# Performance work log

Hardware: AMD Instinct MI355X
Metric: run time of the kernel (lower is better)

Reference implementation:

```python
import jax, jax.numpy as jnp
import numpy as np

B, N, C, K, RPE = 8, 4096, 256, 16, 64
LN_EPS = 1e-5


def _layernorm(x, g, b):
    m = jnp.mean(x, axis=-1, keepdims=True)
    v = jnp.mean((x - m) ** 2, axis=-1, keepdims=True)
    return (x - m) * jax.lax.rsqrt(v + LN_EPS) * g + b


def setup_inputs() -> dict:
    key = jax.random.key(0)
    ks = jax.random.split(key, 10)
    def w(k, shape, s=0.02):
        return jax.random.normal(k, shape, jnp.float32) * s
    return {
        "x": jax.random.normal(ks[0], (B, N, C), jnp.float32),
        "pos": jax.random.normal(ks[1], (B, N, 3), jnp.float32),
        "Wq": w(ks[2], (C, C)),
        "Wk": w(ks[3], (C, C)),
        "Wv": w(ks[4], (C, C)),
        "W1": w(ks[5], (3, RPE)), "b1": jnp.zeros((RPE,), jnp.float32),
        "W2": w(ks[6], (RPE, C)), "b2": jnp.zeros((C,), jnp.float32),
        "Wp": w(ks[7], (C, C)), "bp": jnp.zeros((C,), jnp.float32),
        "gq": jnp.ones((C,), jnp.float32), "betaq": jnp.zeros((C,), jnp.float32),
        "gkv": jnp.ones((C,), jnp.float32), "betakv": jnp.zeros((C,), jnp.float32),
    }


def reference(x, pos, Wq, Wk, Wv, W1, b1, W2, b2, Wp, bp, gq, betaq, gkv, betakv):
    scale = C ** (-0.5)
    x_q = _layernorm(x, gq, betaq)
    x_kv = _layernorm(x, gkv, betakv)
    q = x_q @ Wq                      # (B,N,C)
    k = x_kv @ Wk                     # (B,N,C)
    v = x_kv @ Wv                     # (B,N,C)

    # kNN over squared pairwise distances (self has distance 0 on the diagonal)
    a2 = jnp.sum(pos * pos, axis=-1)                       # (B,N)
    dist2 = a2[:, :, None] + a2[:, None, :] - 2.0 * jnp.einsum(
        "bnc,bmc->bnm", pos, pos)                          # (B,N,N)
    dist2 = jnp.maximum(dist2, 0.0)
    eye = jnp.eye(N, dtype=bool)
    dist2 = jnp.where(eye[None], 0.0, dist2)
    _, idx = jax.lax.top_k(-dist2, K)                      # (B,N,K) smallest-k

    gather = jax.vmap(lambda f, i: f[i])                   # (N,C),(N,K)->(N,K,C)
    k_nb = gather(k, idx)                                  # (B,N,K,C)
    v_nb = gather(v, idx)                                  # (B,N,K,C)
    pos_nb = gather(pos, idx)                              # (B,N,K,3)

    rel = pos[:, :, None, :] - pos_nb                      # (B,N,K,3)
    rel_enc = jax.nn.relu(rel @ W1 + b1) @ W2 + b2         # (B,N,K,C)

    attn_logits = jnp.einsum("bnc,bnkc->bnk", q, k_nb) * scale
    attn_logits = attn_logits + jnp.sum(rel_enc, axis=-1) * scale
    attn = jax.nn.softmax(attn_logits, axis=-1)            # (B,N,K)

    out = jnp.einsum("bnk,bnkc->bnc", attn, v_nb)
    out = out @ Wp + bp
    return out
```

## Files before the change

kernel.cpp:

```cpp
#include <hip/hip_runtime.h>
#include <hip/hip_bf16.h>
#include <stdint.h>

#define Bv 8
#define Nv 4096
#define Cv 256
#define Kv 16
#define RPEv 64
#define CAPv 160

typedef short bf16x8 __attribute__((ext_vector_type(8)));
typedef float f32x4 __attribute__((ext_vector_type(4)));
typedef _Float16 half2v __attribute__((ext_vector_type(2)));
typedef unsigned short u16x2 __attribute__((ext_vector_type(2)));

static __device__ __forceinline__ float bf2f(unsigned int u16) {
    union { unsigned int i; float f; } v; v.i = u16 << 16; return v.f;
}
static __device__ __forceinline__ unsigned short f2bf(float f) {
    union { float f; unsigned int i; } v; v.f = f;
    unsigned int x = v.i;
    return (unsigned short)((x + 0x7fffu + ((x >> 16) & 1u)) >> 16);
}
static __device__ __forceinline__ unsigned int umin32(unsigned int a, unsigned int b) { return a < b ? a : b; }
static __device__ __forceinline__ unsigned int umax32(unsigned int a, unsigned int b) { return a > b ? a : b; }
static __device__ __forceinline__ unsigned short f2h(float f) {
    _Float16 h = (_Float16)f; return __builtin_bit_cast(unsigned short, h);
}
static __device__ __forceinline__ float h2f(unsigned int u) {
    _Float16 h = __builtin_bit_cast(_Float16, (unsigned short)(u & 0xffffu)); return (float)h;
}
static __device__ __forceinline__ half2v bch2(unsigned int u) { return __builtin_bit_cast(half2v, u); }
static __device__ __forceinline__ unsigned int bcu32(u16x2 v) { return __builtin_bit_cast(unsigned int, v); }

__global__ __launch_bounds__(256) void pre_kernel(
    const float* __restrict__ x,
    const float* __restrict__ gq, const float* __restrict__ bq,
    const float* __restrict__ gkv, const float* __restrict__ bkv,
    unsigned short* __restrict__ Aq, unsigned short* __restrict__ Akv,
    const float* __restrict__ Wq, const float* __restrict__ Wk,
    const float* __restrict__ Wv, const float* __restrict__ Wp,
    unsigned short* __restrict__ Bt,
    const float* __restrict__ W2, const float* __restrict__ b2,
    float* __restrict__ w2sum, float* __restrict__ b2sum,
    const float* __restrict__ pos, char* __restrict__ ppos)
{
    const int bid = blockIdx.x;
    const int tid = threadIdx.x;
    if (bid < 4096) {
        const long r0 = (long)bid * 8;
        const int row = tid >> 5;
        const int c0 = (tid & 31) * 8;
        const float* xr = x + (r0 + row) * Cv + c0;
        float xv[8];
        *(float4*)&xv[0] = *(const float4*)xr;
        *(float4*)&xv[4] = *(const float4*)(xr + 4);
        float s = 0.f, s2 = 0.f;
#pragma unroll
        for (int i = 0; i < 8; ++i) { s += xv[i]; s2 = fmaf(xv[i], xv[i], s2); }
#pragma unroll
        for (int m = 16; m >= 1; m >>= 1) { s += __shfl_xor(s, m); s2 += __shfl_xor(s2, m); }
        const float mean = s * (1.f / Cv);
        const float var = fmaf(-mean, mean, s2 * (1.f / Cv));
        const float rs = rsqrtf(fmaxf(var, 0.f) + 1e-5f);
        unsigned int pq[4], pk[4];
#pragma unroll
        for (int i = 0; i < 4; ++i) {
            const int c = c0 + 2 * i;
            const float h0 = (xv[2 * i] - mean) * rs;
            const float h1 = (xv[2 * i + 1] - mean) * rs;
            const unsigned int q0 = f2bf(fmaf(h0, gq[c], bq[c]));
            const unsigned int q1 = f2bf(fmaf(h1, gq[c + 1], bq[c + 1]));
            const unsigned int k0 = f2bf(fmaf(h0, gkv[c], bkv[c]));
            const unsigned int k1 = f2bf(fmaf(h1, gkv[c + 1], bkv[c + 1]));
            pq[i] = q0 | (q1 << 16);
            pk[i] = k0 | (k1 << 16);
        }
        const long off = (r0 + row) * Cv + c0;
        *(uint4*)&Aq[off]  = make_uint4(pq[0], pq[1], pq[2], pq[3]);
        *(uint4*)&Akv[off] = make_uint4(pk[0], pk[1], pk[2], pk[3]);
    } else if (bid < 5120) {
        const int r = bid - 4096;
        const float* W = (r < 256) ? Wq : (r < 512) ? Wk : (r < 768) ? Wv : Wp;
        const int n = r & 255;
        Bt[r * 256 + tid] = f2bf(W[tid * 256 + n]);
    } else if (bid == 5120) {
        if (tid < RPEv) {
            float s = 0.f;
            for (int c = 0; c < Cv; ++c) s += W2[tid * Cv + c];
            w2sum[tid] = s;
        }
        if (tid == 0) {
            float s = 0.f;
            for (int c = 0; c < Cv; ++c) s += b2[c];
            *b2sum = s;
        }
    } else {
        const int b = bid - 5121;
        const float* pb = pos + (size_t)b * Nv * 3;
        uint2* oxy = (uint2*)(ppos + (size_t)b * 24576);
        unsigned int* oz = (unsigned int*)(ppos + (size_t)b * 24576 + 16384);
        for (int i = tid; i < Nv / 2; i += 256) {
            const float* pp = pb + 6 * i;
            const float2 u0 = *(const float2*)pp;
            const float2 u1 = *(const float2*)(pp + 2);
            const float2 u2 = *(const float2*)(pp + 4);
            const unsigned int x0 = f2h(u0.x), y0 = f2h(u0.y), z0 = f2h(u1.x);
            const unsigned int x1 = f2h(u1.y), y1 = f2h(u2.x), z1 = f2h(u2.y);
            oxy[i] = make_uint2(x0 | (x1 << 16), y0 | (y1 << 16));
            oz[i] = z0 | (z1 << 16);
        }
    }
}

__global__ __launch_bounds__(256) void gemm_qkv_kernel(
    const unsigned short* __restrict__ Aq, const unsigned short* __restrict__ Akv,
    const unsigned short* __restrict__ Bt,
    unsigned short* __restrict__ qo, unsigned short* __restrict__ ko,
    unsigned short* __restrict__ vo)
{
    __shared__ unsigned short Albs[2][128 * 64];
    __shared__ unsigned short Blbs[2][128 * 64];

    const int tid = threadIdx.x;
    const int rt = blockIdx.x;
    const int ct = blockIdx.y;
    const unsigned short* A = (ct < 2) ? Aq : Akv;
    const int mat = ct >> 1;
    unsigned short* outp = (mat == 0) ? qo : (mat == 1) ? ko : vo;
    const int colInMat = (ct & 1) * 128;

    const int wid = tid >> 6, l = tid & 63;
    const int wr = wid >> 1, wc = wid & 1;

    int srow[4], scol8[4];
#pragma unroll
    for (int it = 0; it < 4; ++it) {
        const int chunk = it * 256 + tid;
        srow[it] = chunk >> 3;
        scol8[it] = ((chunk & 7) ^ (srow[it] & 7)) * 8;
    }

#define STAGE(buf, ks)                                                                  \
    {                                                                                   \
        _Pragma("unroll")                                                               \
        for (int it = 0; it < 4; ++it) {                                                \
            const unsigned short* ga = A + ((size_t)(rt * 128 + srow[it])) * 256        \
                                         + (ks) * 64 + scol8[it];                       \
            const unsigned short* gb = Bt + ((size_t)(ct * 128 + srow[it])) * 256       \
                                          + (ks) * 64 + scol8[it];                      \
            __builtin_amdgcn_global_load_lds(                                           \
                (const __attribute__((address_space(1))) unsigned int*)(const void*)ga, \
                (__attribute__((address_space(3))) unsigned int*)(void*)                \
                    ((char*)&Albs[buf][0] + (it * 256 + tid) * 16), 16, 0, 0);          \
            __builtin_amdgcn_global_load_lds(                                           \
                (const __attribute__((address_space(1))) unsigned int*)(const void*)gb, \
                (__attribute__((address_space(3))) unsigned int*)(void*)                \
                    ((char*)&Blbs[buf][0] + (it * 256 + tid) * 16), 16, 0, 0);          \
        }                                                                               \
    }

    f32x4 acc[4][4];
#pragma unroll
    for (int m = 0; m < 4; ++m)
#pragma unroll
        for (int n = 0; n < 4; ++n) acc[m][n] = (f32x4){0.f, 0.f, 0.f, 0.f};

    STAGE(0, 0);
    __syncthreads();

    for (int ks = 0; ks < 4; ++ks) {
        const int cur = ks & 1;
        if (ks < 3) STAGE(cur ^ 1, ks + 1);
#pragma unroll
        for (int kk = 0; kk < 2; ++kk) {
            bf16x8 a[4], b[4];
#pragma unroll
            for (int m = 0; m < 4; ++m) {
                const int row = wr * 64 + m * 16 + (l & 15);
                const int byte = row * 128 + ((((kk * 4 + (l >> 4)) * 16)) ^ ((row & 7) << 4));
                a[m] = *(const bf16x8*)((const char*)&Albs[cur][0] + byte);
            }
#pragma unroll
            for (int n = 0; n < 4; ++n) {
                const int row = wc * 64 + n * 16 + (l & 15);
                const int byte = row * 128 + ((((kk * 4 + (l >> 4)) * 16)) ^ ((row & 7) << 4));
                b[n] = *(const bf16x8*)((const char*)&Blbs[cur][0] + byte);
            }
#pragma unroll
            for (int m = 0; m < 4; ++m)
#pragma unroll
                for (int n = 0; n < 4; ++n)
                    acc[m][n] = __builtin_amdgcn_mfma_f32_16x16x32_bf16(a[m], b[n], acc[m][n], 0, 0, 0);
        }
        __syncthreads();
    }

#pragma unroll
    for (int m = 0; m < 4; ++m) {
#pragma unroll
        for (int n = 0; n < 4; ++n) {
#pragma unroll
            for (int j = 0; j < 4; ++j) {
                const int row = rt * 128 + wr * 64 + m * 16 + (l >> 4) * 4 + j;
                const int col = colInMat + wc * 64 + n * 16 + (l & 15);
                outp[(size_t)row * 256 + col] = f2bf(acc[m][n][j]);
            }
        }
    }
#undef STAGE
}

__global__ __launch_bounds__(256) void gemm_proj_kernel(
    const unsigned short* __restrict__ Ab, const unsigned short* __restrict__ Btp,
    const float* __restrict__ bp, float* __restrict__ out)
{
    __shared__ unsigned short Albs[2][128 * 64];
    __shared__ unsigned short Blbs[2][128 * 64];

    const int tid = threadIdx.x;
    const int rt = blockIdx.x;
    const int ct = blockIdx.y;

    const int wid = tid >> 6, l = tid & 63;
    const int wr = wid >> 1, wc = wid & 1;

    int srow[4], scol8[4];
#pragma unroll
    for (int it = 0; it < 4; ++it) {
        const int chunk = it * 256 + tid;
        srow[it] = chunk >> 3;
        scol8[it] = ((chunk & 7) ^ (srow[it] & 7)) * 8;
    }

#define STAGE(buf, ks)                                                                  \
    {                                                                                   \
        _Pragma("unroll")                                                               \
        for (int it = 0; it < 4; ++it) {                                                \
            const unsigned short* ga = Ab + ((size_t)(rt * 128 + srow[it])) * 256       \
                                          + (ks) * 64 + scol8[it];                      \
            const unsigned short* gb = Btp + ((size_t)(ct * 128 + srow[it])) * 256      \
                                           + (ks) * 64 + scol8[it];                     \
            __builtin_amdgcn_global_load_lds(                                           \
                (const __attribute__((address_space(1))) unsigned int*)(const void*)ga, \
                (__attribute__((address_space(3))) unsigned int*)(void*)                \
                    ((char*)&Albs[buf][0] + (it * 256 + tid) * 16), 16, 0, 0);          \
            __builtin_amdgcn_global_load_lds(                                           \
                (const __attribute__((address_space(1))) unsigned int*)(const void*)gb, \
                (__attribute__((address_space(3))) unsigned int*)(void*)                \
                    ((char*)&Blbs[buf][0] + (it * 256 + tid) * 16), 16, 0, 0);          \
        }                                                                               \
    }

    f32x4 acc[4][4];
#pragma unroll
    for (int m = 0; m < 4; ++m)
#pragma unroll
        for (int n = 0; n < 4; ++n) acc[m][n] = (f32x4){0.f, 0.f, 0.f, 0.f};

    STAGE(0, 0);
    __syncthreads();

    for (int ks = 0; ks < 4; ++ks) {
        const int cur = ks & 1;
        if (ks < 3) STAGE(cur ^ 1, ks + 1);
#pragma unroll
        for (int kk = 0; kk < 2; ++kk) {
            bf16x8 a[4], b[4];
#pragma unroll
            for (int m = 0; m < 4; ++m) {
                const int row = wr * 64 + m * 16 + (l & 15);
                const int byte = row * 128 + ((((kk * 4 + (l >> 4)) * 16)) ^ ((row & 7) << 4));
                a[m] = *(const bf16x8*)((const char*)&Albs[cur][0] + byte);
            }
#pragma unroll
            for (int n = 0; n < 4; ++n) {
                const int row = wc * 64 + n * 16 + (l & 15);
                const int byte = row * 128 + ((((kk * 4 + (l >> 4)) * 16)) ^ ((row & 7) << 4));
                b[n] = *(const bf16x8*)((const char*)&Blbs[cur][0] + byte);
            }
#pragma unroll
            for (int m = 0; m < 4; ++m)
#pragma unroll
                for (int n = 0; n < 4; ++n)
                    acc[m][n] = __builtin_amdgcn_mfma_f32_16x16x32_bf16(a[m], b[n], acc[m][n], 0, 0, 0);
        }
        __syncthreads();
    }

#pragma unroll
    for (int n = 0; n < 4; ++n) {
        const int col = ct * 128 + wc * 64 + n * 16 + (l & 15);
        const float bpv = bp[col];
#pragma unroll
        for (int m = 0; m < 4; ++m) {
#pragma unroll
            for (int j = 0; j < 4; ++j) {
                const int row = rt * 128 + wr * 64 + m * 16 + (l >> 4) * 4 + j;
                out[(size_t)row * 256 + col] = acc[m][n][j] + bpv;
            }
        }
    }
#undef STAGE
}

__global__ __launch_bounds__(256) void knn_kernel(
    const float* __restrict__ pos, const char* __restrict__ ppos,
    int* __restrict__ idx_out)
{
    __shared__ char Pbuf[24576];
    __shared__ uint4 qu[32];
    __shared__ unsigned int akeys[256 * 3];
    __shared__ unsigned int cnt[32];
    __shared__ unsigned short bufs[32 * CAPv];

    const uint2* pxy2 = (const uint2*)Pbuf;
    const unsigned int* pz2 = (const unsigned int*)(Pbuf + 16384);

    const int tid = threadIdx.x;
    const int ql = tid >> 3;
    const int s  = tid & 7;
    const int q  = blockIdx.x * 32 + ql;
    const int b  = q >> 12;
    const int n  = q & (Nv - 1);

    {
        const char* src = ppos + (size_t)b * 24576;
#pragma unroll
        for (int it = 0; it < 6; ++it) {
            const int off = (it * 256 + tid) * 16;
            __builtin_amdgcn_global_load_lds(
                (const __attribute__((address_space(1))) unsigned int*)(const void*)(src + off),
                (__attribute__((address_space(3))) unsigned int*)(void*)(Pbuf + off),
                16, 0, 0);
        }
    }
    __syncthreads();

    const int pq = n >> 1;
    const int hq = (n & 1) * 16;
    const uint2 qxy = pxy2[pq];
    const unsigned int qzz = pz2[pq];
    const unsigned int hx = (qxy.x >> hq) & 0xffffu;
    const unsigned int hy = (qxy.y >> hq) & 0xffffu;
    const unsigned int hz = (qzz   >> hq) & 0xffffu;
    const half2v qxp = bch2(hx | (hx << 16));
    const half2v qyp = bch2(hy | (hy << 16));
    const half2v qzp = bch2(hz | (hz << 16));

    u16x2 ch0 = {0x7c00, 0x7c00}, ch1 = ch0, ch2 = ch0;
    for (int t = 0; t < 128; ++t) {
        const int p = 8 * t + s;
        const uint2 xy = pxy2[p];
        const unsigned int zz = pz2[p];
        const half2v dx = bch2(xy.x) - qxp;
        const half2v dy = bch2(xy.y) - qyp;
        const half2v dz = bch2(zz) - qzp;
        const half2v d2 = dx * dx + dy * dy + dz * dz;
        const u16x2 k = __builtin_bit_cast(u16x2, d2);
        const u16x2 mn0 = __builtin_elementwise_min(ch0, k);
        const u16x2 mx0 = __builtin_elementwise_max(ch0, k);
        ch0 = mn0;
        const u16x2 mn1 = __builtin_elementwise_min(ch1, mx0);
        const u16x2 mx1 = __builtin_elementwise_max(ch1, mx0);
        ch1 = mn1;
        ch2 = __builtin_elementwise_min(ch2, mx1);
    }
    akeys[tid * 3 + 0] = bcu32(ch0);
    akeys[tid * 3 + 1] = bcu32(ch1);
    akeys[tid * 3 + 2] = bcu32(ch2);
    __syncthreads();

    if (tid < 32) {
        unsigned int sel16[16];
#pragma unroll
        for (int i = 0; i < 16; ++i) sel16[i] = 0xFFFFFFFFu;
        for (int s8 = 0; s8 < 8; ++s8) {
#pragma unroll
            for (int i3 = 0; i3 < 3; ++i3) {
                const unsigned int v = akeys[(8 * tid + s8) * 3 + i3];
#pragma unroll
                for (int h = 0; h < 2; ++h) {
                    unsigned int cand = (h == 0) ? (v & 0xffffu) : (v >> 16);
                    if (cand < sel16[15]) {
#pragma unroll
                        for (int i = 0; i < 16; ++i) {
                            const unsigned int lo = umin32(sel16[i], cand);
                            cand = umax32(sel16[i], cand);
                            sel16[i] = lo;
                        }
                    }
                }
            }
        }
        const float tauf = h2f(sel16[15]) * 1.12f + 1e-9f;
        const unsigned int taub = f2h(tauf);
        const int n2 = (blockIdx.x * 32 + tid) & (Nv - 1);
        const int pq2 = n2 >> 1;
        const int hq2 = (n2 & 1) * 16;
        const uint2 qxy2 = pxy2[pq2];
        const unsigned int qzz2 = pz2[pq2];
        const unsigned int hx2 = (qxy2.x >> hq2) & 0xffffu;
        const unsigned int hy2 = (qxy2.y >> hq2) & 0xffffu;
        const unsigned int hz2 = (qzz2   >> hq2) & 0xffffu;
        qu[tid] = make_uint4(hx2 | (hx2 << 16), hy2 | (hy2 << 16),
                             hz2 | (hz2 << 16), taub);
        cnt[tid] = 0;
    }
    __syncthreads();

    uint2 cxy[8]; unsigned int czp[8];
#pragma unroll
    for (int k = 0; k < 8; ++k) {
        cxy[k] = pxy2[tid + (k << 8)];
        czp[k] = pz2[tid + (k << 8)];
    }
    for (int q2 = 0; q2 < 32; ++q2) {
        const uint4 Q = qu[q2];
        const half2v Qx = bch2(Q.x), Qy = bch2(Q.y), Qz = bch2(Q.z);
        const unsigned int taub = Q.w;
#pragma unroll
        for (int k = 0; k < 8; ++k) {
            const half2v dx = bch2(cxy[k].x) - Qx;
            const half2v dy = bch2(cxy[k].y) - Qy;
            const half2v dz = bch2(czp[k]) - Qz;
            const half2v d2 = dx * dx + dy * dy + dz * dz;
            const unsigned int bits = __builtin_bit_cast(unsigned int, d2);
            const unsigned int lo = bits & 0xffffu;
            const unsigned int hi = bits >> 16;
            const int p = tid + (k << 8);
            if (lo < taub) {
                const unsigned int slot = atomicAdd(&cnt[q2], 1u);
                if (slot < CAPv) bufs[q2 * CAPv + slot] = (unsigned short)(2 * p);
            }
            if (hi < taub) {
                const unsigned int slot = atomicAdd(&cnt[q2], 1u);
                if (slot < CAPv) bufs[q2 * CAPv + slot] = (unsigned short)(2 * p + 1);
            }
        }
    }
    __syncthreads();

    if (tid < 32) {
        const int q2 = blockIdx.x * 32 + tid;
        const int n2 = q2 & (Nv - 1);
        const int b2 = q2 >> 12;
        const float* pb2 = pos + (size_t)b2 * Nv * 3;
        const double qxd = (double)pb2[3 * n2];
        const double qyd = (double)pb2[3 * n2 + 1];
        const double qzd = (double)pb2[3 * n2 + 2];
        const double a2qd = qxd * qxd + qyd * qyd + qzd * qzd;
        int c = (int)cnt[tid]; if (c > CAPv) c = CAPv;
        unsigned long long sel[Kv];
#pragma unroll
        for (int i = 0; i < Kv; ++i) sel[i] = ~0ull;
        for (int t = 0; t < c; ++t) {
            const int j = bufs[tid * CAPv + t];
            const double cxd = (double)pb2[3 * j];
            const double cyd = (double)pb2[3 * j + 1];
            const double czd = (double)pb2[3 * j + 2];
            const double a2cd = cxd * cxd + cyd * cyd + czd * czd;
            const double ddot = qxd * cxd + qyd * cyd + qzd * czd;
            double dv = (a2qd + a2cd) - 2.0 * ddot;
            dv = (dv < 0.0) ? 0.0 : dv;
            if (j == n2) dv = 0.0;
            union { double d; unsigned long long u; } cv; cv.d = dv;
            const unsigned long long key = (cv.u & ~0xFFFULL) | (unsigned long long)j;
            if (key < sel[Kv - 1]) {
                unsigned long long cc = key;
#pragma unroll
                for (int i = 0; i < Kv; ++i) {
                    const unsigned long long lo = (sel[i] < cc) ? sel[i] : cc;
                    const unsigned long long hi = (sel[i] < cc) ? cc : sel[i];
                    sel[i] = lo; cc = hi;
                }
            }
        }
#pragma unroll
        for (int i = 0; i < Kv; ++i)
            idx_out[(long)q2 * Kv + i] = (int)(sel[i] & 0xFFFull);
    }
}

__global__ __launch_bounds__(256) void attn_core_kernel(
    unsigned short* __restrict__ qb, const unsigned short* __restrict__ kb,
    const unsigned short* __restrict__ vb, const int* __restrict__ idx,
    const float* __restrict__ pos, const float* __restrict__ W1,
    const float* __restrict__ b1, const float* __restrict__ w2sum,
    const float* __restrict__ b2sum)
{
    __shared__ float q_lds[8][Cv];
    __shared__ float lg[8][Kv];
    __shared__ float wgt[8][Kv];
    __shared__ int idx_l[8][Kv];
    __shared__ float W1l[3 * RPEv];
    __shared__ float b1l[RPEv], w2s[RPEv];
    __shared__ float posq[24];
    __shared__ float b2s_l;

    const int tid = threadIdx.x;
    const long r0 = (long)blockIdx.x * 8;
    const int bq = (int)(r0 >> 12);

    {
        float* ql = &q_lds[0][0];
        for (int i = tid; i < 8 * Cv; i += 256) ql[i] = bf2f(qb[r0 * Cv + i]);
    }
    if (tid < 128) ((int*)idx_l)[tid] = idx[r0 * Kv + tid];
    if (tid < 3 * RPEv) W1l[tid] = W1[tid];
    if (tid < RPEv) { b1l[tid] = b1[tid]; w2s[tid] = w2sum[tid]; }
    if (tid < 24) posq[tid] = pos[r0 * 3 + tid];
    if (tid == 0) b2s_l = *b2sum;
    __syncthreads();

    const int g = tid >> 4, l = tid & 15;
    for (int r = 0; r < 8; ++r) {
        const int nb = idx_l[r][g];
        const long gi = (long)bq * Nv + nb;
        const unsigned short* kr = kb + gi * Cv + l * 16;
        const float* qq = &q_lds[r][l * 16];
        const uint4 kA = *(const uint4*)kr;
        const uint4 kB = *(const uint4*)(kr + 8);
        float part = 0.f;
        part = fmaf(qq[0],  bf2f(kA.x & 0xffffu), part);
        part = fmaf(qq[1],  bf2f(kA.x >> 16),     part);
        part = fmaf(qq[2],  bf2f(kA.y & 0xffffu), part);
        part = fmaf(qq[3],  bf2f(kA.y >> 16),     part);
        part = fmaf(qq[4],  bf2f(kA.z & 0xffffu), part);
        part = fmaf(qq[5],  bf2f(kA.z >> 16),     part);
        part = fmaf(qq[6],  bf2f(kA.w & 0xffffu), part);
        part = fmaf(qq[7],  bf2f(kA.w >> 16),     part);
        part = fmaf(qq[8],  bf2f(kB.x & 0xffffu), part);
        part = fmaf(qq[9],  bf2f(kB.x >> 16),     part);
        part = fmaf(qq[10], bf2f(kB.y & 0xffffu), part);
        part = fmaf(qq[11], bf2f(kB.y >> 16),     part);
        part = fmaf(qq[12], bf2f(kB.z & 0xffffu), part);
        part = fmaf(qq[13], bf2f(kB.z >> 16),     part);
        part = fmaf(qq[14], bf2f(kB.w & 0xffffu), part);
        part = fmaf(qq[15], bf2f(kB.w >> 16),     part);
        const float rx = posq[r * 3 + 0] - pos[gi * 3 + 0];
        const float ry = posq[r * 3 + 1] - pos[gi * 3 + 1];
        const float rz = posq[r * 3 + 2] - pos[gi * 3 + 2];
#pragma unroll
        for (int u4 = 0; u4 < 4; ++u4) {
            const int u = l * 4 + u4;
            float h = fmaf(rx, W1l[u], fmaf(ry, W1l[RPEv + u], fmaf(rz, W1l[2 * RPEv + u], b1l[u])));
            h = fmaxf(h, 0.f);
            part = fmaf(h, w2s[u], part);
        }
        part += __shfl_xor(part, 8);
        part += __shfl_xor(part, 4);
        part += __shfl_xor(part, 2);
        part += __shfl_xor(part, 1);
        if (l == 0) lg[r][g] = (part + b2s_l) * 0.0625f;
    }
    __syncthreads();
    if (tid < 128) {
        const int rr = tid >> 4, gg = tid & 15;
        const float v = lg[rr][gg];
        float m = v;
        m = fmaxf(m, __shfl_xor(m, 8)); m = fmaxf(m, __shfl_xor(m, 4));
        m = fmaxf(m, __shfl_xor(m, 2)); m = fmaxf(m, __shfl_xor(m, 1));
        const float e = __expf(v - m);
        float ssum = e;
        ssum += __shfl_xor(ssum, 8); ssum += __shfl_xor(ssum, 4);
        ssum += __shfl_xor(ssum, 2); ssum += __shfl_xor(ssum, 1);
        wgt[rr][gg] = e / ssum;
    }
    __syncthreads();
    {
        const int c = tid;
        for (int r = 0; r < 8; ++r) {
            float acc = 0.f;
#pragma unroll
            for (int t = 0; t < Kv; ++t) {
                const long gi = (long)bq * Nv + idx_l[r][t];
                acc = fmaf(wgt[r][t], bf2f((unsigned)vb[gi * Cv + c]), acc);
            }
            qb[(r0 + r) * Cv + c] = f2bf(acc);
        }
    }
}

extern "C" void kernel_launch(void* const* d_in, const int* in_sizes, int n_in,
                              void* d_out, int out_size, void* d_ws, size_t ws_size,
                              hipStream_t stream) {
    (void)in_sizes; (void)n_in; (void)out_size; (void)ws_size;
    const float* x      = (const float*)d_in[0];
    const float* pos    = (const float*)d_in[1];
    const float* Wq     = (const float*)d_in[2];
    const float* Wk     = (const float*)d_in[3];
    const float* Wv     = (const float*)d_in[4];
    const float* W1     = (const float*)d_in[5];
    const float* b1     = (const float*)d_in[6];
    const float* W2     = (const float*)d_in[7];
    const float* b2     = (const float*)d_in[8];
    const float* Wp     = (const float*)d_in[9];
    const float* bp     = (const float*)d_in[10];
    const float* gq     = (const float*)d_in[11];
    const float* betaq  = (const float*)d_in[12];
    const float* gkv    = (const float*)d_in[13];
    const float* betakv = (const float*)d_in[14];
    float* out = (float*)d_out;

    char* ws = (char*)d_ws;
    unsigned short* qb = (unsigned short*)(ws);
    unsigned short* kb = (unsigned short*)(ws + 16777216);
    unsigned short* vb = (unsigned short*)(ws + 33554432);
    int*   idx   = (int*)  (ws + 50331648);
    unsigned short* Bt = (unsigned short*)(ws + 52428800);
    float* w2sum = (float*)(ws + 52953088);
    float* b2sum = (float*)(ws + 52953344);
    char*  ppos  = ws + 52953600;

    unsigned short* Aq  = (unsigned short*)d_out;
    unsigned short* Akv = (unsigned short*)d_out + 8388608;

    hipLaunchKernelGGL(pre_kernel, dim3(5129), dim3(256), 0, stream,
                       x, gq, betaq, gkv, betakv, Aq, Akv,
                       Wq, Wk, Wv, Wp, Bt, W2, b2, w2sum, b2sum, pos, ppos);
    hipLaunchKernelGGL(gemm_qkv_kernel, dim3(256, 6), dim3(256), 0, stream,
                       Aq, Akv, Bt, qb, kb, vb);
    hipLaunchKernelGGL(knn_kernel, dim3(1024), dim3(256), 0, stream, pos, ppos, idx);
    hipLaunchKernelGGL(attn_core_kernel, dim3(4096), dim3(256), 0, stream,
                       qb, kb, vb, idx, pos, W1, b1, w2sum, b2sum);
    hipLaunchKernelGGL(gemm_proj_kernel, dim3(256, 2), dim3(256), 0, stream,
                       qb, Bt + 768 * 256, bp, out);
}
```

Baseline: 222.0 us.

## Merge kNN search and QKV GEMM into one heterogeneous-block kernel launch

Combines the kNN kernel and the QKV GEMM kernel into a single launch: the first 1024 blocks run the kNN search and the remaining blocks run the MFMA GEMM, so the compute-heavy search can overlap the GEMM. Each kNN block now converts the positions to packed fp16 directly into LDS, which removes the separate packing pass in pre_kernel and its global round trip. The coarse threshold pass also now scans all 2048 packed pairs instead of 1024, which adds work. The merged kernel reserves 64 KB of LDS for every block, which may lower occupancy for the kNN blocks.

```diff
diff --git a/kernel.cpp b/kernel.cpp
--- a/kernel.cpp
+++ b/kernel.cpp
@@ -42,8 +42,7 @@
     const float* __restrict__ Wv, const float* __restrict__ Wp,
     unsigned short* __restrict__ Bt,
     const float* __restrict__ W2, const float* __restrict__ b2,
-    float* __restrict__ w2sum, float* __restrict__ b2sum,
-    const float* __restrict__ pos, char* __restrict__ ppos)
+    float* __restrict__ w2sum, float* __restrict__ b2sum)
 {
     const int bid = blockIdx.x;
     const int tid = threadIdx.x;
@@ -84,7 +83,7 @@
         const float* W = (r < 256) ? Wq : (r < 512) ? Wk : (r < 768) ? Wv : Wp;
         const int n = r & 255;
         Bt[r * 256 + tid] = f2bf(W[tid * 256 + n]);
-    } else if (bid == 5120) {
+    } else {
         if (tid < RPEv) {
             float s = 0.f;
             for (int c = 0; c < Cv; ++c) s += W2[tid * Cv + c];
@@ -95,11 +94,35 @@
             for (int c = 0; c < Cv; ++c) s += b2[c];
             *b2sum = s;
         }
-    } else {
-        const int b = bid - 5121;
+    }
+}
+
+__global__ __launch_bounds__(256) void gemmknn_kernel(
+    const float* __restrict__ pos, int* __restrict__ idx_out,
+    const unsigned short* __restrict__ Aq, const unsigned short* __restrict__ Akv,
+    const unsigned short* __restrict__ Bt,
+    unsigned short* __restrict__ qo, unsigned short* __restrict__ ko,
+    unsigned short* __restrict__ vo)
+{
+    __shared__ char smem[65536] __attribute__((aligned(16)));
+    const int tid = threadIdx.x;
+    const int bid = blockIdx.x;
+
+    if (bid < 1024) {
+        uint2* pxy2 = (uint2*)smem;
+        unsigned int* pz2 = (unsigned int*)(smem + 16384);
+        uint4* qu = (uint4*)(smem + 24576);
+        unsigned int* akeys = (unsigned int*)(smem + 25088);
+        unsigned int* cnt = (unsigned int*)(smem + 28160);
+        unsigned short* bufs = (unsigned short*)(smem + 28288);
+
+        const int ql = tid >> 3;
+        const int s  = tid & 7;
+        const int q  = bid * 32 + ql;
+        const int b  = q >> 12;
+        const int n  = q & (Nv - 1);
         const float* pb = pos + (size_t)b * Nv * 3;
-        uint2* oxy = (uint2*)(ppos + (size_t)b * 24576);
-        unsigned int* oz = (unsigned int*)(ppos + (size_t)b * 24576 + 16384);
+
         for (int i = tid; i < Nv / 2; i += 256) {
             const float* pp = pb + 6 * i;
             const float2 u0 = *(const float2*)pp;
@@ -107,39 +130,179 @@
             const float2 u2 = *(const float2*)(pp + 4);
             const unsigned int x0 = f2h(u0.x), y0 = f2h(u0.y), z0 = f2h(u1.x);
             const unsigned int x1 = f2h(u1.y), y1 = f2h(u2.x), z1 = f2h(u2.y);
-            oxy[i] = make_uint2(x0 | (x1 << 16), y0 | (y1 << 16));
-            oz[i] = z0 | (z1 << 16);
-        }
-    }
-}
-
-__global__ __launch_bounds__(256) void gemm_qkv_kernel(
-    const unsigned short* __restrict__ Aq, const unsigned short* __restrict__ Akv,
-    const unsigned short* __restrict__ Bt,
-    unsigned short* __restrict__ qo, unsigned short* __restrict__ ko,
-    unsigned short* __restrict__ vo)
-{
-    __shared__ unsigned short Albs[2][128 * 64];
-    __shared__ unsigned short Blbs[2][128 * 64];
-
-    const int tid = threadIdx.x;
-    const int rt = blockIdx.x;
-    const int ct = blockIdx.y;
-    const unsigned short* A = (ct < 2) ? Aq : Akv;
-    const int mat = ct >> 1;
-    unsigned short* outp = (mat == 0) ? qo : (mat == 1) ? ko : vo;
-    const int colInMat = (ct & 1) * 128;
-
-    const int wid = tid >> 6, l = tid & 63;
-    const int wr = wid >> 1, wc = wid & 1;
-
-    int srow[4], scol8[4];
-#pragma unroll
-    for (int it = 0; it < 4; ++it) {
-        const int chunk = it * 256 + tid;
-        srow[it] = chunk >> 3;
-        scol8[it] = ((chunk & 7) ^ (srow[it] & 7)) * 8;
-    }
+            pxy2[i] = make_uint2(x0 | (x1 << 16), y0 | (y1 << 16));
+            pz2[i] = z0 | (z1 << 16);
+        }
+        __syncthreads();
+
+        const int pq = n >> 1;
+        const int hq = (n & 1) * 16;
+        const uint2 qxy = pxy2[pq];
+        const unsigned int qzz = pz2[pq];
+        const unsigned int hx = (qxy.x >> hq) & 0xffffu;
+        const unsigned int hy = (qxy.y >> hq) & 0xffffu;
+        const unsigned int hz = (qzz   >> hq) & 0xffffu;
+        const half2v qxp = bch2(hx | (hx << 16));
+        const half2v qyp = bch2(hy | (hy << 16));
+        const half2v qzp = bch2(hz | (hz << 16));
+
+        u16x2 ch0 = {0x7c00, 0x7c00}, ch1 = ch0, ch2 = ch0;
+        for (int t = 0; t < 256; ++t) {
+            const int p = 8 * t + s;
+            const uint2 xy = pxy2[p];
+            const unsigned int zz = pz2[p];
+            const half2v dx = bch2(xy.x) - qxp;
+            const half2v dy = bch2(xy.y) - qyp;
+            const half2v dz = bch2(zz) - qzp;
+            const half2v d2 = dx * dx + dy * dy + dz * dz;
+            const u16x2 k = __builtin_bit_cast(u16x2, d2);
+            const u16x2 mn0 = __builtin_elementwise_min(ch0, k);
+            const u16x2 mx0 = __builtin_elementwise_max(ch0, k);
+            ch0 = mn0;
+            const u16x2 mn1 = __builtin_elementwise_min(ch1, mx0);
+            const u16x2 mx1 = __builtin_elementwise_max(ch1, mx0);
+            ch1 = mn1;
+            ch2 = __builtin_elementwise_min(ch2, mx1);
+        }
+        akeys[tid * 3 + 0] = bcu32(ch0);
+        akeys[tid * 3 + 1] = bcu32(ch1);
+        akeys[tid * 3 + 2] = bcu32(ch2);
+        __syncthreads();
+
+        if (tid < 32) {
+            unsigned int sel16[16];
+#pragma unroll
+            for (int i = 0; i < 16; ++i) sel16[i] = 0xFFFFFFFFu;
+            for (int s8 = 0; s8 < 8; ++s8) {
+#pragma unroll
+                for (int i3 = 0; i3 < 3; ++i3) {
+                    const unsigned int v = akeys[(8 * tid + s8) * 3 + i3];
+#pragma unroll
+                    for (int h = 0; h < 2; ++h) {
+                        unsigned int cand = (h == 0) ? (v & 0xffffu) : (v >> 16);
+                        if (cand < sel16[15]) {
+#pragma unroll
+                            for (int i = 0; i < 16; ++i) {
+                                const unsigned int lo = umin32(sel16[i], cand);
+                                cand = umax32(sel16[i], cand);
+                                sel16[i] = lo;
+                            }
+                        }
+                    }
+                }
+            }
+            const float tauf = h2f(sel16[15]) * 1.12f + 1e-9f;
+            const unsigned int taub = f2h(tauf);
+            const int n2 = (bid * 32 + tid) & (Nv - 1);
+            const int pq2 = n2 >> 1;
+            const int hq2 = (n2 & 1) * 16;
+            const uint2 qxy2 = pxy2[pq2];
+            const unsigned int qzz2 = pz2[pq2];
+            const unsigned int hx2 = (qxy2.x >> hq2) & 0xffffu;
+            const unsigned int hy2 = (qxy2.y >> hq2) & 0xffffu;
+            const unsigned int hz2 = (qzz2   >> hq2) & 0xffffu;
+            qu[tid] = make_uint4(hx2 | (hx2 << 16), hy2 | (hy2 << 16),
+                                 hz2 | (hz2 << 16), taub);
+            cnt[tid] = 0;
+        }
+        __syncthreads();
+
+        uint2 cxy[8]; unsigned int czp[8];
+#pragma unroll
+        for (int k = 0; k < 8; ++k) {
+            cxy[k] = pxy2[tid + (k << 8)];
+            czp[k] = pz2[tid + (k << 8)];
+        }
+        for (int q2 = 0; q2 < 32; ++q2) {
+            const uint4 Q = qu[q2];
+            const half2v Qx = bch2(Q.x), Qy = bch2(Q.y), Qz = bch2(Q.z);
+            const unsigned int taub = Q.w;
+#pragma unroll
+            for (int k = 0; k < 8; ++k) {
+                const half2v dx = bch2(cxy[k].x) - Qx;
+                const half2v dy = bch2(cxy[k].y) - Qy;
+                const half2v dz = bch2(czp[k]) - Qz;
+                const half2v d2 = dx * dx + dy * dy + dz * dz;
+                const unsigned int bits = __builtin_bit_cast(unsigned int, d2);
+                const unsigned int lo = bits & 0xffffu;
+                const unsigned int hi = bits >> 16;
+                const int p = tid + (k << 8);
+                if (lo < taub) {
+                    const unsigned int slot = atomicAdd(&cnt[q2], 1u);
+                    if (slot < CAPv) bufs[q2 * CAPv + slot] = (unsigned short)(2 * p);
+                }
+                if (hi < taub) {
+                    const unsigned int slot = atomicAdd(&cnt[q2], 1u);
+                    if (slot < CAPv) bufs[q2 * CAPv + slot] = (unsigned short)(2 * p + 1);
+                }
+            }
+        }
+        __syncthreads();
+
+        if (tid < 32) {
+            const int q2 = bid * 32 + tid;
+            const int n2 = q2 & (Nv - 1);
+            const int b2 = q2 >> 12;
+            const float* pb2 = pos + (size_t)b2 * Nv * 3;
+            const double qxd = (double)pb2[3 * n2];
+            const double qyd = (double)pb2[3 * n2 + 1];
+            const double qzd = (double)pb2[3 * n2 + 2];
+            const double a2qd = qxd * qxd + qyd * qyd + qzd * qzd;
+            int c = (int)cnt[tid]; if (c > CAPv) c = CAPv;
+            unsigned long long sel[Kv];
+#pragma unroll
+            for (int i = 0; i < Kv; ++i) sel[i] = ~0ull;
+            for (int t = 0; t < c; ++t) {
+                const int j = bufs[tid * CAPv + t];
+                const double cxd = (double)pb2[3 * j];
+                const double cyd = (double)pb2[3 * j + 1];
+                const double czd = (double)pb2[3 * j + 2];
+                const double a2cd = cxd * cxd + cyd * cyd + czd * czd;
+                const double ddot = qxd * cxd + qyd * cyd + qzd * czd;
+                double dv = (a2qd + a2cd) - 2.0 * ddot;
+                dv = (dv < 0.0) ? 0.0 : dv;
+                if (j == n2) dv = 0.0;
+                union { double d; unsigned long long u; } cv; cv.d = dv;
+                const unsigned long long key = (cv.u & ~0xFFFULL) | (unsigned long long)j;
+                if (key < sel[Kv - 1]) {
+                    unsigned long long cc = key;
+#pragma unroll
+                    for (int i = 0; i < Kv; ++i) {
+                        const unsigned long long lo = (sel[i] < cc) ? sel[i] : cc;
+                        const unsigned long long hi = (sel[i] < cc) ? cc : sel[i];
+                        sel[i] = lo; cc = hi;
+                    }
+                }
+            }
+#pragma unroll
+            for (int i = 0; i < Kv; ++i)
+                idx_out[(long)q2 * Kv + i] = (int)(sel[i] & 0xFFFull);
+        }
+        return;
+    }
+
+    {
+        unsigned short (*Albs)[128 * 64] = (unsigned short (*)[128 * 64])smem;
+        unsigned short (*Blbs)[128 * 64] = (unsigned short (*)[128 * 64])(smem + 32768);
+
+        const int gb = bid - 1024;
+        const int rt = gb & 255;
+        const int ct = gb >> 8;
+        const unsigned short* A = (ct < 2) ? Aq : Akv;
+        const int mat = ct >> 1;
+        unsigned short* outp = (mat == 0) ? qo : (mat == 1) ? ko : vo;
+        const int colInMat = (ct & 1) * 128;
+
+        const int wid = tid >> 6, l = tid & 63;
+        const int wr = wid >> 1, wc = wid & 1;
+
+        int srow[4], scol8[4];
+#pragma unroll
+        for (int it = 0; it < 4; ++it) {
+            const int chunk = it * 256 + tid;
+            srow[it] = chunk >> 3;
+            scol8[it] = ((chunk & 7) ^ (srow[it] & 7)) * 8;
+        }
 
 #define STAGE(buf, ks)                                                                  \
     {                                                                                   \
@@ -147,68 +310,69 @@
         for (int it = 0; it < 4; ++it) {                                                \
             const unsigned short* ga = A + ((size_t)(rt * 128 + srow[it])) * 256        \
                                          + (ks) * 64 + scol8[it];                       \
-            const unsigned short* gb = Bt + ((size_t)(ct * 128 + srow[it])) * 256       \
-                                          + (ks) * 64 + scol8[it];                      \
+            const unsigned short* gb_ = Bt + ((size_t)(ct * 128 + srow[it])) * 256      \
+                                           + (ks) * 64 + scol8[it];                     \
             __builtin_amdgcn_global_load_lds(                                           \
                 (const __attribute__((address_space(1))) unsigned int*)(const void*)ga, \
                 (__attribute__((address_space(3))) unsigned int*)(void*)                \
                     ((char*)&Albs[buf][0] + (it * 256 + tid) * 16), 16, 0, 0);          \
             __builtin_amdgcn_global_load_lds(                                           \
-                (const __attribute__((address_space(1))) unsigned int*)(const void*)gb, \
+                (const __attribute__((address_space(1))) unsigned int*)(const void*)gb_,\
                 (__attribute__((address_space(3))) unsigned int*)(void*)                \
                     ((char*)&Blbs[buf][0] + (it * 256 + tid) * 16), 16, 0, 0);          \
         }                                                                               \
     }
 
-    f32x4 acc[4][4];
-#pragma unroll
-    for (int m = 0; m < 4; ++m)
-#pragma unroll
-        for (int n = 0; n < 4; ++n) acc[m][n] = (f32x4){0.f, 0.f, 0.f, 0.f};
-
-    STAGE(0, 0);
-    __syncthreads();
-
-    for (int ks = 0; ks < 4; ++ks) {
-        const int cur = ks & 1;
-        if (ks < 3) STAGE(cur ^ 1, ks + 1);
-#pragma unroll
-        for (int kk = 0; kk < 2; ++kk) {
-            bf16x8 a[4], b[4];
-#pragma unroll
-            for (int m = 0; m < 4; ++m) {
-                const int row = wr * 64 + m * 16 + (l & 15);
-                const int byte = row * 128 + ((((kk * 4 + (l >> 4)) * 16)) ^ ((row & 7) << 4));
-                a[m] = *(const bf16x8*)((const char*)&Albs[cur][0] + byte);
-            }
+        f32x4 acc[4][4];
+#pragma unroll
+        for (int m = 0; m < 4; ++m)
+#pragma unroll
+            for (int n = 0; n < 4; ++n) acc[m][n] = (f32x4){0.f, 0.f, 0.f, 0.f};
+
+        STAGE(0, 0);
+        __syncthreads();
+
+        for (int ks = 0; ks < 4; ++ks) {
+            const int cur = ks & 1;
+            if (ks < 3) STAGE(cur ^ 1, ks + 1);
+#pragma unroll
+            for (int kk = 0; kk < 2; ++kk) {
+                bf16x8 a[4], b[4];
+#pragma unroll
+                for (int m = 0; m < 4; ++m) {
+                    const int row = wr * 64 + m * 16 + (l & 15);
+                    const int byte = row * 128 + ((((kk * 4 + (l >> 4)) * 16)) ^ ((row & 7) << 4));
+                    a[m] = *(const bf16x8*)((const char*)&Albs[cur][0] + byte);
+                }
+#pragma unroll
+                for (int n = 0; n < 4; ++n) {
+                    const int row = wc * 64 + n * 16 + (l & 15);
+                    const int byte = row * 128 + ((((kk * 4 + (l >> 4)) * 16)) ^ ((row & 7) << 4));
+                    b[n] = *(const bf16x8*)((const char*)&Blbs[cur][0] + byte);
+                }
+#pragma unroll
+                for (int m = 0; m < 4; ++m)
+#pragma unroll
+                    for (int n = 0; n < 4; ++n)
+                        acc[m][n] = __builtin_amdgcn_mfma_f32_16x16x32_bf16(a[m], b[n], acc[m][n], 0, 0, 0);
+            }
+            __syncthreads();
+        }
+
+#pragma unroll
+        for (int m = 0; m < 4; ++m) {
 #pragma unroll
             for (int n = 0; n < 4; ++n) {
-                const int row = wc * 64 + n * 16 + (l & 15);
-                const int byte = row * 128 + ((((kk * 4 + (l >> 4)) * 16)) ^ ((row & 7) << 4));
-                b[n] = *(const bf16x8*)((const char*)&Blbs[cur][0] + byte);
-            }
-#pragma unroll
-            for (int m = 0; m < 4; ++m)
-#pragma unroll
-                for (int n = 0; n < 4; ++n)
-                    acc[m][n] = __builtin_amdgcn_mfma_f32_16x16x32_bf16(a[m], b[n], acc[m][n], 0, 0, 0);
-        }
-        __syncthreads();
-    }
-
-#pragma unroll
-    for (int m = 0; m < 4; ++m) {
-#pragma unroll
-        for (int n = 0; n < 4; ++n) {
-#pragma unroll
-            for (int j = 0; j < 4; ++j) {
-                const int row = rt * 128 + wr * 64 + m * 16 + (l >> 4) * 4 + j;
-                const int col = colInMat + wc * 64 + n * 16 + (l & 15);
-                outp[(size_t)row * 256 + col] = f2bf(acc[m][n][j]);
-            }
-        }
-    }
+#pragma unroll
+                for (int j = 0; j < 4; ++j) {
+                    const int row = rt * 128 + wr * 64 + m * 16 + (l >> 4) * 4 + j;
+                    const int col = colInMat + wc * 64 + n * 16 + (l & 15);
+                    outp[(size_t)row * 256 + col] = f2bf(acc[m][n][j]);
+                }
+            }
+        }
 #undef STAGE
+    }
 }
 
 __global__ __launch_bounds__(256) void gemm_proj_kernel(
@@ -302,184 +466,6 @@
         }
     }
 #undef STAGE
-}
-
-__global__ __launch_bounds__(256) void knn_kernel(
-    const float* __restrict__ pos, const char* __restrict__ ppos,
-    int* __restrict__ idx_out)
-{
-    __shared__ char Pbuf[24576];
-    __shared__ uint4 qu[32];
-    __shared__ unsigned int akeys[256 * 3];
-    __shared__ unsigned int cnt[32];
-    __shared__ unsigned short bufs[32 * CAPv];
-
-    const uint2* pxy2 = (const uint2*)Pbuf;
-    const unsigned int* pz2 = (const unsigned int*)(Pbuf + 16384);
-
-    const int tid = threadIdx.x;
-    const int ql = tid >> 3;
-    const int s  = tid & 7;
-    const int q  = blockIdx.x * 32 + ql;
-    const int b  = q >> 12;
-    const int n  = q & (Nv - 1);
-
-    {
-        const char* src = ppos + (size_t)b * 24576;
-#pragma unroll
-        for (int it = 0; it < 6; ++it) {
-            const int off = (it * 256 + tid) * 16;
-            __builtin_amdgcn_global_load_lds(
-                (const __attribute__((address_space(1))) unsigned int*)(const void*)(src + off),
-                (__attribute__((address_space(3))) unsigned int*)(void*)(Pbuf + off),
-                16, 0, 0);
-        }
-    }
-    __syncthreads();
-
-    const int pq = n >> 1;
-    const int hq = (n & 1) * 16;
-    const uint2 qxy = pxy2[pq];
-    const unsigned int qzz = pz2[pq];
-    const unsigned int hx = (qxy.x >> hq) & 0xffffu;
-    const unsigned int hy = (qxy.y >> hq) & 0xffffu;
-    const unsigned int hz = (qzz   >> hq) & 0xffffu;
-    const half2v qxp = bch2(hx | (hx << 16));
-    const half2v qyp = bch2(hy | (hy << 16));
-    const half2v qzp = bch2(hz | (hz << 16));
-
-    u16x2 ch0 = {0x7c00, 0x7c00}, ch1 = ch0, ch2 = ch0;
-    for (int t = 0; t < 128; ++t) {
-        const int p = 8 * t + s;
-        const uint2 xy = pxy2[p];
-        const unsigned int zz = pz2[p];
-        const half2v dx = bch2(xy.x) - qxp;
-        const half2v dy = bch2(xy.y) - qyp;
-        const half2v dz = bch2(zz) - qzp;
-        const half2v d2 = dx * dx + dy * dy + dz * dz;
-        const u16x2 k = __builtin_bit_cast(u16x2, d2);
-        const u16x2 mn0 = __builtin_elementwise_min(ch0, k);
-        const u16x2 mx0 = __builtin_elementwise_max(ch0, k);
-        ch0 = mn0;
-        const u16x2 mn1 = __builtin_elementwise_min(ch1, mx0);
-        const u16x2 mx1 = __builtin_elementwise_max(ch1, mx0);
-        ch1 = mn1;
-        ch2 = __builtin_elementwise_min(ch2, mx1);
-    }
-    akeys[tid * 3 + 0] = bcu32(ch0);
-    akeys[tid * 3 + 1] = bcu32(ch1);
-    akeys[tid * 3 + 2] = bcu32(ch2);
-    __syncthreads();
-
-    if (tid < 32) {
-        unsigned int sel16[16];
-#pragma unroll
-        for (int i = 0; i < 16; ++i) sel16[i] = 0xFFFFFFFFu;
-        for (int s8 = 0; s8 < 8; ++s8) {
-#pragma unroll
-            for (int i3 = 0; i3 < 3; ++i3) {
-                const unsigned int v = akeys[(8 * tid + s8) * 3 + i3];
-#pragma unroll
-                for (int h = 0; h < 2; ++h) {
-                    unsigned int cand = (h == 0) ? (v & 0xffffu) : (v >> 16);
-                    if (cand < sel16[15]) {
-#pragma unroll
-                        for (int i = 0; i < 16; ++i) {
-                            const unsigned int lo = umin32(sel16[i], cand);
-                            cand = umax32(sel16[i], cand);
-                            sel16[i] = lo;
-                        }
-                    }
-                }
-            }
-        }
-        const float tauf = h2f(sel16[15]) * 1.12f + 1e-9f;
-        const unsigned int taub = f2h(tauf);
-        const int n2 = (blockIdx.x * 32 + tid) & (Nv - 1);
-        const int pq2 = n2 >> 1;
-        const int hq2 = (n2 & 1) * 16;
-        const uint2 qxy2 = pxy2[pq2];
-        const unsigned int qzz2 = pz2[pq2];
-        const unsigned int hx2 = (qxy2.x >> hq2) & 0xffffu;
-        const unsigned int hy2 = (qxy2.y >> hq2) & 0xffffu;
-        const unsigned int hz2 = (qzz2   >> hq2) & 0xffffu;
-        qu[tid] = make_uint4(hx2 | (hx2 << 16), hy2 | (hy2 << 16),
-                             hz2 | (hz2 << 16), taub);
-        cnt[tid] = 0;
-    }
-    __syncthreads();
-
-    uint2 cxy[8]; unsigned int czp[8];
-#pragma unroll
-    for (int k = 0; k < 8; ++k) {
-        cxy[k] = pxy2[tid + (k << 8)];
-        czp[k] = pz2[tid + (k << 8)];
-    }
-    for (int q2 = 0; q2 < 32; ++q2) {
-        const uint4 Q = qu[q2];
-        const half2v Qx = bch2(Q.x), Qy = bch2(Q.y), Qz = bch2(Q.z);
-        const unsigned int taub = Q.w;
-#pragma unroll
-        for (int k = 0; k < 8; ++k) {
-            const half2v dx = bch2(cxy[k].x) - Qx;
-            const half2v dy = bch2(cxy[k].y) - Qy;
-            const half2v dz = bch2(czp[k]) - Qz;
-            const half2v d2 = dx * dx + dy * dy + dz * dz;
-            const unsigned int bits = __builtin_bit_cast(unsigned int, d2);
-            const unsigned int lo = bits & 0xffffu;
-            const unsigned int hi = bits >> 16;
-            const int p = tid + (k << 8);
-            if (lo < taub) {
-                const unsigned int slot = atomicAdd(&cnt[q2], 1u);
-                if (slot < CAPv) bufs[q2 * CAPv + slot] = (unsigned short)(2 * p);
-            }
-            if (hi < taub) {
-                const unsigned int slot = atomicAdd(&cnt[q2], 1u);
-                if (slot < CAPv) bufs[q2 * CAPv + slot] = (unsigned short)(2 * p + 1);
-            }
-        }
-    }
-    __syncthreads();
-
-    if (tid < 32) {
-        const int q2 = blockIdx.x * 32 + tid;
-        const int n2 = q2 & (Nv - 1);
-        const int b2 = q2 >> 12;
-        const float* pb2 = pos + (size_t)b2 * Nv * 3;
-        const double qxd = (double)pb2[3 * n2];
-        const double qyd = (double)pb2[3 * n2 + 1];
-        const double qzd = (double)pb2[3 * n2 + 2];
-        const double a2qd = qxd * qxd + qyd * qyd + qzd * qzd;
-        int c = (int)cnt[tid]; if (c > CAPv) c = CAPv;
-        unsigned long long sel[Kv];
-#pragma unroll
-        for (int i = 0; i < Kv; ++i) sel[i] = ~0ull;
-        for (int t = 0; t < c; ++t) {
-            const int j = bufs[tid * CAPv + t];
-            const double cxd = (double)pb2[3 * j];
-            const double cyd = (double)pb2[3 * j + 1];
-            const double czd = (double)pb2[3 * j + 2];
-            const double a2cd = cxd * cxd + cyd * cyd + czd * czd;
-            const double ddot = qxd * cxd + qyd * cyd + qzd * czd;
-            double dv = (a2qd + a2cd) - 2.0 * ddot;
-            dv = (dv < 0.0) ? 0.0 : dv;
-            if (j == n2) dv = 0.0;
-            union { double d; unsigned long long u; } cv; cv.d = dv;
-            const unsigned long long key = (cv.u & ~0xFFFULL) | (unsigned long long)j;
-            if (key < sel[Kv - 1]) {
-                unsigned long long cc = key;
-#pragma unroll
-                for (int i = 0; i < Kv; ++i) {
-                    const unsigned long long lo = (sel[i] < cc) ? sel[i] : cc;
-                    const unsigned long long hi = (sel[i] < cc) ? cc : sel[i];
-                    sel[i] = lo; cc = hi;
-                }
-            }
-        }
-#pragma unroll
-        for (int i = 0; i < Kv; ++i)
-            idx_out[(long)q2 * Kv + i] = (int)(sel[i] & 0xFFFull);
-    }
 }
 
 __global__ __launch_bounds__(256) void attn_core_kernel(
@@ -611,17 +597,15 @@
     unsigned short* Bt = (unsigned short*)(ws + 52428800);
     float* w2sum = (float*)(ws + 52953088);
     float* b2sum = (float*)(ws + 52953344);
-    char*  ppos  = ws + 52953600;
 
     unsigned short* Aq  = (unsigned short*)d_out;
     unsigned short* Akv = (unsigned short*)d_out + 8388608;
 
-    hipLaunchKernelGGL(pre_kernel, dim3(5129), dim3(256), 0, stream,
+    hipLaunchKernelGGL(pre_kernel, dim3(5121), dim3(256), 0, stream,
                        x, gq, betaq, gkv, betakv, Aq, Akv,
-                       Wq, Wk, Wv, Wp, Bt, W2, b2, w2sum, b2sum, pos, ppos);
-    hipLaunchKernelGGL(gemm_qkv_kernel, dim3(256, 6), dim3(256), 0, stream,
-                       Aq, Akv, Bt, qb, kb, vb);
-    hipLaunchKernelGGL(knn_kernel, dim3(1024), dim3(256), 0, stream, pos, ppos, idx);
+                       Wq, Wk, Wv, Wp, Bt, W2, b2, w2sum, b2sum);
+    hipLaunchKernelGGL(gemmknn_kernel, dim3(2560), dim3(256), 0, stream,
+                       pos, idx, Aq, Akv, Bt, qb, kb, vb);
     hipLaunchKernelGGL(attn_core_kernel, dim3(4096), dim3(256), 0, stream,
                        qb, kb, vb, idx, pos, W1, b1, w2sum, b2sum);
     hipLaunchKernelGGL(gemm_proj_kernel, dim3(256, 2), dim3(256), 0, stream,
```

Measured after the change: 230.5 us. 1.04x slower.
